# Optimization experiments

Measured on AMD Instinct MI355X. Metric: run time of the kernel, lower is better.

The kernel has to match this reference:

```python
import jax, jax.numpy as jnp
import numpy as np

BS, N, M, D = 4, 8192, 8192, 3

def setup_inputs() -> dict:
    key = jax.random.key(0)
    k1, k2 = jax.random.split(key)
    preds = jax.random.normal(k1, (BS, M, D), dtype=jnp.float32)
    gts = jax.random.normal(k2, (BS, N, D), dtype=jnp.float32)
    mask = jnp.ones((BS, M), dtype=jnp.float32)
    return {"preds": preds, "gts": gts, "mask": mask}

def _pairwise_dist(x, y):
    # x: [bs, N, d] (gts), y: [bs, M, d] (preds)
    # P[b,n,m] = ||x_n||^2 + ||y_m||^2 - 2 x_n . y_m
    rx = jnp.sum(x * x, axis=-1)            # [bs, N] (diag of x @ x^T)
    ry = jnp.sum(y * y, axis=-1)            # [bs, M] (diag of y @ y^T)
    zz = jnp.einsum('bnd,bmd->bnm', x, y)   # [bs, N, M]
    return rx[:, :, None] + ry[:, None, :] - 2.0 * zz

def reference(preds, gts, mask):
    P = _pairwise_dist(gts, preds)          # [bs, N, M]; mask unused (as in source)
    return (jnp.min(P, axis=1),             # [bs, M] min over gts for each pred
            jnp.min(P, axis=2),             # [bs, N] min over preds for each gt
            jnp.argmin(P, axis=1),          # [bs, M]
            jnp.argmin(P, axis=2))          # [bs, N]
```

## Files before the change

kernel.cpp:

```cpp
#include <hip/hip_runtime.h>

#pragma clang fp contract(off)


#define BS     4
#define NPTS   8192
#define CHUNK  1024
#define BLOCK  1024
#define SPLITS 32
#define SLOTS  32
#define QT     4
#define QBLK   (SLOTS * QT)
#define ROWS   (CHUNK / SPLITS)

typedef float f32x2 __attribute__((ext_vector_type(2)));

__global__ __launch_bounds__(BLOCK, 8)
void chamfer_kernel(const float* __restrict__ preds,
                    const float* __restrict__ gts,
                    float* __restrict__ out)
{
#pragma clang fp contract(off)
    const int dir   = blockIdx.z;
    const int b     = blockIdx.y;
    const int t     = threadIdx.x;
    const int slot  = t & (SLOTS - 1);
    const int split = t >> 5;
    const int qb    = blockIdx.x * QBLK;

    const float* qbase = (dir == 0 ? preds : gts) + (size_t)b * NPTS * 3;
    const float* rbase = (dir == 0 ? gts : preds) + (size_t)b * NPTS * 3;
    float* outv = out + (size_t)dir       * BS * NPTS + (size_t)b * NPTS;
    float* outi = out + (size_t)(2 + dir) * BS * NPTS + (size_t)b * NPTS;

    f32x2 qxv[2], qyv[2], qzv[2], rqv[2];
#pragma unroll
    for (int g = 0; g < 2; ++g) {
#pragma unroll
        for (int h = 0; h < 2; ++h) {
            const int j = g * 2 + h;
            const int q = qb + j * SLOTS + slot;
            const float x = qbase[(size_t)q * 3 + 0];
            const float y = qbase[(size_t)q * 3 + 1];
            const float z = qbase[(size_t)q * 3 + 2];
            qxv[g][h] = x; qyv[g][h] = y; qzv[g][h] = z;
            const float a0 = x * x;
            const float a1 = y * y;
            const float a2 = z * z;
            rqv[g][h] = (a0 + a1) + a2;
        }
    }

    __shared__ float sh[CHUNK][4];
    __shared__ float shv[SPLITS][SLOTS];
    __shared__ int   shi[SPLITS][SLOTS];

    float bestv[QT];
    int   besti[QT];
#pragma unroll
    for (int j = 0; j < QT; ++j) { bestv[j] = 3.0e38f; besti[j] = 0; }

    const int nchunks = NPTS / CHUNK;
    for (int c = 0; c < nchunks; ++c) {
        __syncthreads();
        {
            const size_t n = (size_t)c * CHUNK + t;
            const float x = rbase[n * 3 + 0];
            const float y = rbase[n * 3 + 1];
            const float z = rbase[n * 3 + 2];
            sh[t][0] = x;
            sh[t][1] = y;
            sh[t][2] = z;
            const float a0 = x * x;
            const float a1 = y * y;
            const float a2 = z * z;
            sh[t][3] = (a0 + a1) + a2;
        }
        __syncthreads();

        const int row0 = split * ROWS;
#pragma unroll 4
        for (int k = 0; k < ROWS; ++k) {
            const int row = row0 + k;
            const float x  = sh[row][0];
            const float y  = sh[row][1];
            const float z  = sh[row][2];
            const float rr = sh[row][3];
            const int idx = c * CHUNK + row;
#pragma unroll
            for (int g = 0; g < 2; ++g) {
                const f32x2 p0 = qxv[g] * x;
                const f32x2 p1 = qyv[g] * y;
                const f32x2 p2 = qzv[g] * z;
                const f32x2 zz = (p0 + p1) + p2;
                const f32x2 ts = rqv[g] + rr;
                const f32x2 w  = zz * 2.0f;
                const f32x2 v  = ts - w;
                if (v[0] < bestv[2 * g + 0]) { bestv[2 * g + 0] = v[0]; besti[2 * g + 0] = idx; }
                if (v[1] < bestv[2 * g + 1]) { bestv[2 * g + 1] = v[1]; besti[2 * g + 1] = idx; }
            }
        }
    }

#pragma unroll
    for (int j = 0; j < QT; ++j) {
        __syncthreads();
        shv[split][slot] = bestv[j];
        shi[split][slot] = besti[j];
        __syncthreads();
        if (t < SLOTS) {
            float bv = shv[0][t];
            int   bi = shi[0][t];
            for (int s = 1; s < SPLITS; ++s) {
                const float v2 = shv[s][t];
                const int   i2 = shi[s][t];
                if (v2 < bv || (v2 == bv && i2 < bi)) { bv = v2; bi = i2; }
            }
            const int q = qb + j * SLOTS + t;
            outv[q] = bv;
            outi[q] = (float)bi;
        }
    }
}

extern "C" void kernel_launch(void* const* d_in, const int* in_sizes, int n_in,
                              void* d_out, int out_size, void* d_ws, size_t ws_size,
                              hipStream_t stream)
{
    const float* preds = (const float*)d_in[0];
    const float* gts   = (const float*)d_in[1];
    float* out = (float*)d_out;

    dim3 grid(NPTS / QBLK, BS, 2);
    dim3 block(BLOCK);
    chamfer_kernel<<<grid, block, 0, stream>>>(preds, gts, out);
}
```

Baseline: 126.4 us.

## Double queries per thread and parallelize the final split reduction

Each thread now holds 8 query points instead of 4, so every reference point loaded from shared memory is reused across twice as many distance computations and the grid has half as many blocks. The cross-split reduction is rewritten: all partial minima are written to shared memory at once, with indices packed as 16-bit, and reduced by all threads using a 4-way shuffle. This replaces the old serial loop run by 32 threads. More registers per thread lowers the launch-bounds occupancy target, and the shared buffer is reused by aliasing it across phases.

```diff
diff --git a/kernel.cpp b/kernel.cpp
--- a/kernel.cpp
+++ b/kernel.cpp
@@ -9,13 +9,13 @@
 #define BLOCK  1024
 #define SPLITS 32
 #define SLOTS  32
-#define QT     4
+#define QT     8
 #define QBLK   (SLOTS * QT)
 #define ROWS   (CHUNK / SPLITS)
 
 typedef float f32x2 __attribute__((ext_vector_type(2)));
 
-__global__ __launch_bounds__(BLOCK, 8)
+__global__ __launch_bounds__(BLOCK, 4)
 void chamfer_kernel(const float* __restrict__ preds,
                     const float* __restrict__ gts,
                     float* __restrict__ out)
@@ -33,9 +33,14 @@
     float* outv = out + (size_t)dir       * BS * NPTS + (size_t)b * NPTS;
     float* outi = out + (size_t)(2 + dir) * BS * NPTS + (size_t)b * NPTS;
 
-    f32x2 qxv[2], qyv[2], qzv[2], rqv[2];
+    __shared__ float smem[12288];
+    float (*sh)[4]        = (float (*)[4])smem;
+    float *shv            = smem;
+    unsigned short *shi16 = (unsigned short *)(smem + 8192);
+
+    f32x2 qxv[4], qyv[4], qzv[4], rqv[4];
 #pragma unroll
-    for (int g = 0; g < 2; ++g) {
+    for (int g = 0; g < 4; ++g) {
 #pragma unroll
         for (int h = 0; h < 2; ++h) {
             const int j = g * 2 + h;
@@ -50,10 +55,6 @@
             rqv[g][h] = (a0 + a1) + a2;
         }
     }
-
-    __shared__ float sh[CHUNK][4];
-    __shared__ float shv[SPLITS][SLOTS];
-    __shared__ int   shi[SPLITS][SLOTS];
 
     float bestv[QT];
     int   besti[QT];
@@ -88,7 +89,7 @@
             const float rr = sh[row][3];
             const int idx = c * CHUNK + row;
 #pragma unroll
-            for (int g = 0; g < 2; ++g) {
+            for (int g = 0; g < 4; ++g) {
                 const f32x2 p0 = qxv[g] * x;
                 const f32x2 p1 = qyv[g] * y;
                 const f32x2 p2 = qzv[g] * z;
@@ -102,24 +103,34 @@
         }
     }
 
+    __syncthreads();
 #pragma unroll
     for (int j = 0; j < QT; ++j) {
-        __syncthreads();
-        shv[split][slot] = bestv[j];
-        shi[split][slot] = besti[j];
-        __syncthreads();
-        if (t < SLOTS) {
-            float bv = shv[0][t];
-            int   bi = shi[0][t];
-            for (int s = 1; s < SPLITS; ++s) {
-                const float v2 = shv[s][t];
-                const int   i2 = shi[s][t];
-                if (v2 < bv || (v2 == bv && i2 < bi)) { bv = v2; bi = i2; }
-            }
-            const int q = qb + j * SLOTS + t;
-            outv[q] = bv;
-            outi[q] = (float)bi;
-        }
+        shv  [split * QBLK + j * SLOTS + slot] = bestv[j];
+        shi16[split * QBLK + j * SLOTS + slot] = (unsigned short)besti[j];
+    }
+    __syncthreads();
+
+    const int qloc = t >> 2;
+    const int sl   = t & 3;
+    float bv = 3.0e38f;
+    int   bi = 0;
+#pragma unroll
+    for (int k = 0; k < SPLITS / 4; ++k) {
+        const int s = sl + k * 4;
+        const float v2 = shv[s * QBLK + qloc];
+        const int   i2 = shi16[s * QBLK + qloc];
+        if (v2 < bv || (v2 == bv && i2 < bi)) { bv = v2; bi = i2; }
+    }
+#pragma unroll
+    for (int o = 1; o < 4; o <<= 1) {
+        const float ov = __shfl_xor(bv, o);
+        const int   oi = __shfl_xor(bi, o);
+        if (ov < bv || (ov == bv && oi < bi)) { bv = ov; bi = oi; }
+    }
+    if (sl == 0) {
+        outv[qb + qloc] = bv;
+        outi[qb + qloc] = (float)bi;
     }
 }
 
```

After: 117.9 us. -6.8%, faster.
